# Kernel optimization log

Measured on AMD Instinct MI355X. Metric: run time of the kernel, lower is better.

## Reference

```python
import jax, jax.numpy as jnp
import numpy as np

DIM = 256
HEADS = 8
HEAD_DIM = DIM // HEADS
WS = 8
EPS = 1e-5


def layernorm(x, g, b):
    mu = jnp.mean(x, axis=-1, keepdims=True)
    var = jnp.var(x, axis=-1, keepdims=True)
    return (x - mu) * jax.lax.rsqrt(var + EPS) * g + b


def partition_windows(x, ws):
    B, H, W, C = x.shape
    x = x.reshape(B, H // ws, ws, W // ws, ws, C)
    x = jnp.transpose(x, (0, 1, 3, 2, 4, 5))
    return x.reshape(B * (H // ws) * (W // ws), ws * ws, C)


def unpartition_windows(x, ws, B, H, W):
    C = x.shape[-1]
    x = x.reshape(B, H // ws, W // ws, ws, ws, C)
    x = jnp.transpose(x, (0, 1, 3, 2, 4, 5))
    return x.reshape(B, H, W, C)


def setup_inputs() -> dict:
    key = jax.random.key(0)
    ks = jax.random.split(key, 14)
    B, H, W, C = 16, 64, 64, DIM
    s_in = 1.0 / np.sqrt(C)
    s_hid = 1.0 / np.sqrt(4 * C)
    return {
        "x": jax.random.normal(ks[0], (B, H, W, C), jnp.float32),
        "ln1_g": jnp.ones((C,), jnp.float32),
        "ln1_b": jnp.zeros((C,), jnp.float32),
        "qkv_w": jax.random.uniform(ks[1], (3 * C, C), jnp.float32, -s_in, s_in),
        "qkv_b": jax.random.uniform(ks[2], (3 * C,), jnp.float32, -s_in, s_in),
        "proj_w": jax.random.uniform(ks[3], (C, C), jnp.float32, -s_in, s_in),
        "proj_b": jax.random.uniform(ks[4], (C,), jnp.float32, -s_in, s_in),
        "ln2_g": jnp.ones((C,), jnp.float32),
        "ln2_b": jnp.zeros((C,), jnp.float32),
        "ffn_w1": jax.random.uniform(ks[5], (4 * C, C), jnp.float32, -s_in, s_in),
        "ffn_b1": jax.random.uniform(ks[6], (4 * C,), jnp.float32, -s_in, s_in),
        "ffn_w2": jax.random.uniform(ks[7], (C, 4 * C), jnp.float32, -s_hid, s_hid),
        "ffn_b2": jax.random.uniform(ks[8], (C,), jnp.float32, -s_hid, s_hid),
    }


def attention(blocks, qkv_w, qkv_b, proj_w, proj_b):
    # blocks: [Bn, N, C]
    Bn, N, C = blocks.shape
    qkv = blocks @ qkv_w.T + qkv_b  # [Bn, N, 3C]
    qkv = qkv.reshape(Bn, N, 3, HEADS, HEAD_DIM)
    q, k, v = qkv[:, :, 0], qkv[:, :, 1], qkv[:, :, 2]  # each [Bn, N, h, d]
    # Faithful to the source: q @ k^T over the last two dims -> head-x-head scores per token
    scores = jnp.einsum("bnhd,bngd->bnhg", q, k) / np.sqrt(HEAD_DIM)
    attn = jax.nn.softmax(scores, axis=-1)
    out = jnp.einsum("bnhg,bngd->bnhd", attn, v).reshape(Bn, N, C)
    return out @ proj_w.T + proj_b


def reference(x, ln1_g, ln1_b, qkv_w, qkv_b, proj_w, proj_b,
              ln2_g, ln2_b, ffn_w1, ffn_b1, ffn_w2, ffn_b2):
    B, H, W, C = x.shape
    x_ = layernorm(x, ln1_g, ln1_b)
    blocks = partition_windows(x_, WS)  # [B*nW, ws*ws, C]
    out = attention(blocks, qkv_w, qkv_b, proj_w, proj_b)
    x = x + unpartition_windows(out, WS, B, H, W)
    x_ = layernorm(x, ln2_g, ln2_b)
    x_ = jax.nn.relu(x_ @ ffn_w1.T + ffn_b1) @ ffn_w2.T + ffn_b2
    return x + x_
```

## Files before the change

### kernel.cpp

```cpp
#include <hip/hip_runtime.h>
#include <hip/hip_bf16.h>
#include <stdint.h>

typedef float f32x4 __attribute__((ext_vector_type(4)));
typedef __bf16 bf16x8 __attribute__((ext_vector_type(8)));
typedef unsigned short ushort8 __attribute__((ext_vector_type(8)));

__device__ __forceinline__ float bf2f(unsigned short u) {
    unsigned int x = ((unsigned int)u) << 16;
    return __builtin_bit_cast(float, x);
}
__device__ __forceinline__ unsigned short f2bf(float f) {
    unsigned int x = __builtin_bit_cast(unsigned int, f);
    unsigned int lsb = (x >> 16) & 1u;
    x += 0x7fffu + lsb;
    return (unsigned short)(x >> 16);
}

#define GLL16(gptr, lptr)                                                      \
    __builtin_amdgcn_global_load_lds(                                          \
        (const __attribute__((address_space(1))) void*)(gptr),                 \
        (__attribute__((address_space(3))) void*)(lptr), 16, 0, 0)

__global__ __launch_bounds__(256) void cvt4_kernel(
    const float* __restrict__ w0, const float* __restrict__ w1,
    const float* __restrict__ w2, const float* __restrict__ w3,
    unsigned short* __restrict__ dst)
{
    const int i = blockIdx.x * 256 + threadIdx.x;
    const float* s; int off;
    if      (i <  49152) { s = w0; off = 0; }
    else if (i <  65536) { s = w1; off = 49152; }
    else if (i < 131072) { s = w2; off = 65536; }
    else                 { s = w3; off = 131072; }
    f32x4 v = ((const f32x4*)s)[i - off];
    ushort4 o;
    o.x = f2bf(v.x); o.y = f2bf(v.y); o.z = f2bf(v.z); o.w = f2bf(v.w);
    ((ushort4*)dst)[i] = o;
}

__global__ __launch_bounds__(256) void ln_kernel(
    const float* __restrict__ x, const float* __restrict__ g,
    const float* __restrict__ b, unsigned short* __restrict__ y)
{
    const int lane = threadIdx.x & 63, wave = threadIdx.x >> 6;
    const size_t tok = (size_t)blockIdx.x * 4 + wave;
    f32x4 v = *(const f32x4*)(x + tok * 256 + lane * 4);
    float s = v.x + v.y + v.z + v.w;
    float q = v.x * v.x + v.y * v.y + v.z * v.z + v.w * v.w;
#pragma unroll
    for (int o = 32; o; o >>= 1) {
        s += __shfl_xor(s, o, 64);
        q += __shfl_xor(q, o, 64);
    }
    float mean = s * (1.f / 256.f);
    float var  = q * (1.f / 256.f) - mean * mean;
    float rstd = rsqrtf(var + 1e-5f);
    f32x4 gr = *(const f32x4*)(g + lane * 4);
    f32x4 br = *(const f32x4*)(b + lane * 4);
    ushort4 o4;
    o4.x = f2bf((v.x - mean) * rstd * gr.x + br.x);
    o4.y = f2bf((v.y - mean) * rstd * gr.y + br.y);
    o4.z = f2bf((v.z - mean) * rstd * gr.z + br.z);
    o4.w = f2bf((v.w - mean) * rstd * gr.w + br.w);
    *(ushort4*)(y + tok * 256 + lane * 4) = o4;
}

template <int RELU, int HASRES, int OUTF32>
__global__ __launch_bounds__(256) void gemm_bt(
    const unsigned short* __restrict__ A,
    const unsigned short* __restrict__ W,
    const float* __restrict__ bias,
    const float* res,
    void* Cv,
    int M, int N, int K, int nby)
{
    __shared__ __align__(16) unsigned short As[128 * 64];
    __shared__ __align__(16) unsigned short Bs[128 * 64];

    const int t    = threadIdx.x;
    const int id   = blockIdx.x;
    const int xcd  = id & 7;
    const int sl   = id >> 3;
    const int by   = sl % nby;
    const int bx   = (sl / nby) * 8 + xcd;
    const int m0   = bx * 128;
    const int n0   = by * 128;
    const int lane = t & 63;
    const int wave = t >> 6;
    const int wm = wave & 1, wn = wave >> 1;
    const int lr = lane & 15, kc = lane >> 4;

    f32x4 acc[4][4] = {};

    const int rA   = t >> 3;
    const int gcol = ((t & 7) ^ (rA & 7)) * 8;
    const unsigned short* gA = A + (size_t)(m0 + rA) * K + gcol;
    const unsigned short* gB = W + (size_t)(n0 + rA) * K + gcol;

    for (int k0 = 0; k0 < K; k0 += 64) {
#pragma unroll
        for (int w = 0; w < 4; ++w) {
            GLL16(gA + (size_t)(w * 32) * K + k0, &As[(w * 256 + t) * 8]);
            GLL16(gB + (size_t)(w * 32) * K + k0, &Bs[(w * 256 + t) * 8]);
        }
        __syncthreads();

#pragma unroll
        for (int hh = 0; hh < 2; ++hh) {
            bf16x8 af[4], bf[4];
#pragma unroll
            for (int i = 0; i < 4; ++i) {
                const int ra = wm * 64 + i * 16 + lr;
                const int rb = wn * 64 + i * 16 + lr;
                af[i] = *(const bf16x8*)&As[ra * 64 + ((hh * 4 + kc) ^ (ra & 7)) * 8];
                bf[i] = *(const bf16x8*)&Bs[rb * 64 + ((hh * 4 + kc) ^ (rb & 7)) * 8];
            }
#pragma unroll
            for (int i = 0; i < 4; ++i)
#pragma unroll
                for (int j = 0; j < 4; ++j)
                    acc[i][j] = __builtin_amdgcn_mfma_f32_16x16x32_bf16(
                        af[i], bf[j], acc[i][j], 0, 0, 0);
        }
        __syncthreads();
    }

    float* Cf = (float*)Cv;
    unsigned short* Cb = (unsigned short*)Cv;
    const int row0 = m0 + wm * 64;
    const int col0 = n0 + wn * 64;
    const int cl = lane & 15;
    const int rq = (lane >> 4) * 4;
#pragma unroll
    for (int i = 0; i < 4; ++i) {
#pragma unroll
        for (int j = 0; j < 4; ++j) {
            const int col = col0 + j * 16 + cl;
            const float bv = bias[col];
#pragma unroll
            for (int r = 0; r < 4; ++r) {
                const int row = row0 + i * 16 + rq + r;
                float v = acc[i][j][r] + bv;
                if (RELU) v = fmaxf(v, 0.f);
                const size_t o = (size_t)row * N + col;
                if (HASRES) v += res[o];
                if (OUTF32) Cf[o] = v;
                else        Cb[o] = f2bf(v);
            }
        }
    }
}

__global__ __launch_bounds__(512, 2) void proj_attn(
    const unsigned short* __restrict__ qkv,
    const unsigned short* __restrict__ wp,
    const float* __restrict__ bias,
    const float* __restrict__ res,
    float* __restrict__ out)
{
    __shared__ __align__(16) unsigned short U[128 * 256];
    __shared__ __align__(16) unsigned short Wk[2][16384];

    const int t = threadIdx.x;
    const int lane = t & 63, wave = t >> 6;
    const int m0 = blockIdx.x * 128;
    const int lr = lane & 15, kc = lane >> 4;
    const int cl = lane & 15, rq = (lane >> 4) * 4;
    const int wm = wave & 1, wn = wave >> 1;

    const int r2b = t >> 3;
    const int gc2 = (t & 7) ^ (r2b & 7);

    #define STAGE_WP(kc4, Wt)                                                  \
        do {                                                                   \
            _Pragma("unroll")                                                  \
            for (int j = 0; j < 4; ++j)                                        \
                GLL16(wp + (size_t)(j * 64 + r2b) * 256 + (kc4) * 64 + gc2 * 8,\
                      &(Wt)[(j * 512 + t) * 8]);                               \
        } while (0)

    STAGE_WP(0, Wk[0]);
    STAGE_WP(1, Wk[1]);

    const int h = lane >> 3, g = lane & 7;
    for (int p = 0; p < 16; ++p) {
        const int row = p * 8 + wave;
        const unsigned short* base = qkv + (size_t)(m0 + row) * 768;

        float s = 0.f;
#pragma unroll
        for (int d8 = 0; d8 < 4; ++d8) {
            ushort4 qa = *(const ushort4*)(base + h * 32 + d8 * 8);
            ushort4 qb = *(const ushort4*)(base + h * 32 + d8 * 8 + 4);
            ushort4 ka = *(const ushort4*)(base + 256 + g * 32 + d8 * 8);
            ushort4 kb = *(const ushort4*)(base + 256 + g * 32 + d8 * 8 + 4);
            s += bf2f(qa.x) * bf2f(ka.x) + bf2f(qa.y) * bf2f(ka.y)
               + bf2f(qa.z) * bf2f(ka.z) + bf2f(qa.w) * bf2f(ka.w)
               + bf2f(qb.x) * bf2f(kb.x) + bf2f(qb.y) * bf2f(kb.y)
               + bf2f(qb.z) * bf2f(kb.z) + bf2f(qb.w) * bf2f(kb.w);
        }
        s *= 0.17677669529663687f;

        float mx = s;
#pragma unroll
        for (int o = 1; o < 8; o <<= 1) mx = fmaxf(mx, __shfl_xor(mx, o, 64));
        float e = __expf(s - mx);
        float sum = e;
#pragma unroll
        for (int o = 1; o < 8; o <<= 1) sum += __shfl_xor(sum, o, 64);
        const float a = e / sum;

        float o0 = 0.f, o1 = 0.f, o2 = 0.f, o3 = 0.f;
#pragma unroll
        for (int gg = 0; gg < 8; ++gg) {
            const float ag = __shfl(a, (lane & 56) | gg, 64);
            ushort4 vv = *(const ushort4*)(base + 512 + gg * 32 + g * 4);
            o0 += ag * bf2f(vv.x);
            o1 += ag * bf2f(vv.y);
            o2 += ag * bf2f(vv.z);
            o3 += ag * bf2f(vv.w);
        }
        const int gcu = lane >> 1;
        const int sc = (gcu & ~7) | ((gcu & 7) ^ (row & 7));
        ushort4 ov;
        ov.x = f2bf(o0); ov.y = f2bf(o1); ov.z = f2bf(o2); ov.w = f2bf(o3);
        *(ushort4*)&U[row * 256 + sc * 8 + (lane & 1) * 4] = ov;
    }
    __syncthreads();

    bf16x8 afr[4][8];
#pragma unroll
    for (int i = 0; i < 4; ++i) {
        const int ra = wm * 64 + i * 16 + lr;
#pragma unroll
        for (int ks = 0; ks < 8; ++ks) {
            const int c = ks * 4 + kc;
            afr[i][ks] = *(const bf16x8*)
                &U[ra * 256 + ((c & ~7) | ((c & 7) ^ (ra & 7))) * 8];
        }
    }

    f32x4 acc[4][4] = {};
    for (int c4 = 0; c4 < 4; ++c4) {
        if (c4 >= 2) __syncthreads();
        const unsigned short* Wc = Wk[c4 & 1];
#pragma unroll
        for (int kk = 0; kk < 2; ++kk) {
            const int c = kk * 4 + kc;
            bf16x8 bw[4];
#pragma unroll
            for (int j = 0; j < 4; ++j) {
                const int rb = wn * 64 + j * 16 + lr;
                bw[j] = *(const bf16x8*)&Wc[rb * 64 + ((c ^ (rb & 7)) * 8)];
            }
#pragma unroll
            for (int i = 0; i < 4; ++i)
#pragma unroll
                for (int j = 0; j < 4; ++j)
                    acc[i][j] = __builtin_amdgcn_mfma_f32_16x16x32_bf16(
                        afr[i][c4 * 2 + kk], bw[j], acc[i][j], 0, 0, 0);
        }
        if (c4 < 2) {
            __syncthreads();
            STAGE_WP(c4 + 2, Wk[c4 & 1]);
        }
    }

#pragma unroll
    for (int i = 0; i < 4; ++i)
#pragma unroll
        for (int j = 0; j < 4; ++j) {
            const int col = wn * 64 + j * 16 + cl;
            const float bv = bias[col];
#pragma unroll
            for (int r = 0; r < 4; ++r) {
                const int row = m0 + wm * 64 + i * 16 + rq + r;
                const size_t o = (size_t)row * 256 + col;
                out[o] = acc[i][j][r] + bv + res[o];
            }
        }
    #undef STAGE_WP
}

__global__ __launch_bounds__(512, 2) void ffn_fused(
    float* xo,
    const float* __restrict__ ln2_g, const float* __restrict__ ln2_b,
    const unsigned short* __restrict__ w1,
    const float* __restrict__ b1p,
    const unsigned short* __restrict__ w2,
    const float* __restrict__ b2p)
{
    __shared__ __align__(16) unsigned short U[32768];
    __shared__ __align__(16) unsigned short W1a[16384];
    __shared__ __align__(16) unsigned short W2a[16384];
    __shared__ __align__(16) unsigned short Hs[2][8192];

    unsigned short* const W1b = U;
    unsigned short* const W2b = U + 16384;

    const int t = threadIdx.x;
    const int lane = t & 63, wave = t >> 6;
    const int m0 = blockIdx.x * 128;
    const int lr = lane & 15, kc = lane >> 4;
    const int cl = lane & 15, rq = (lane >> 4) * 4;
    const int wm = wave & 1, wn = wave >> 1;

    const int r1b = t >> 5;
    const int sc1 = t & 31;
    const int gc1 = (sc1 & ~7) | ((sc1 & 7) ^ (r1b & 7));
    const int r2b = t >> 3;
    const int gc2 = (t & 7) ^ (r2b & 7);

    #define STAGE_W1(hp, W1t)                                                  \
        do {                                                                   \
            _Pragma("unroll")                                                  \
            for (int j = 0; j < 4; ++j)                                        \
                GLL16(w1 + (size_t)((hp) * 64 + j * 16 + r1b) * 256 + gc1 * 8, \
                      &(W1t)[(j * 512 + t) * 8]);                              \
        } while (0)
    #define STAGE_W2(hp, W2t)                                                  \
        do {                                                                   \
            _Pragma("unroll")                                                  \
            for (int j = 0; j < 4; ++j)                                        \
                GLL16(w2 + (size_t)(j * 64 + r2b) * 1024 + (hp) * 64 + gc2 * 8,\
                      &(W2t)[(j * 512 + t) * 8]);                              \
        } while (0)

    STAGE_W1(0, W1a);
    STAGE_W2(0, W2a);

    {
        const int row0 = t >> 2;
        const int seg  = t & 3;
        const float* xrp = xo + (size_t)(m0 + row0) * 256 + seg * 64;
        f32x4 xv[16];
#pragma unroll
        for (int i = 0; i < 16; ++i) xv[i] = ((const f32x4*)xrp)[i];
        float s = 0.f, q = 0.f;
#pragma unroll
        for (int i = 0; i < 16; ++i) {
            s += xv[i].x + xv[i].y + xv[i].z + xv[i].w;
            q += xv[i].x * xv[i].x + xv[i].y * xv[i].y
               + xv[i].z * xv[i].z + xv[i].w * xv[i].w;
        }
        s += __shfl_xor(s, 1, 64); q += __shfl_xor(q, 1, 64);
        s += __shfl_xor(s, 2, 64); q += __shfl_xor(q, 2, 64);
        const float mean = s * (1.f / 256.f);
        const float rstd = rsqrtf(q * (1.f / 256.f) - mean * mean + 1e-5f);
#pragma unroll
        for (int c8 = 0; c8 < 8; ++c8) {
            const f32x4 g0 = ((const f32x4*)(ln2_g + seg * 64 + c8 * 8))[0];
            const f32x4 g1 = ((const f32x4*)(ln2_g + seg * 64 + c8 * 8))[1];
            const f32x4 bb0 = ((const f32x4*)(ln2_b + seg * 64 + c8 * 8))[0];
            const f32x4 bb1 = ((const f32x4*)(ln2_b + seg * 64 + c8 * 8))[1];
            const f32x4 a0 = xv[c8 * 2], a1 = xv[c8 * 2 + 1];
            ushort8 o;
            o[0] = f2bf((a0.x - mean) * rstd * g0.x + bb0.x);
            o[1] = f2bf((a0.y - mean) * rstd * g0.y + bb0.y);
            o[2] = f2bf((a0.z - mean) * rstd * g0.z + bb0.z);
            o[3] = f2bf((a0.w - mean) * rstd * g0.w + bb0.w);
            o[4] = f2bf((a1.x - mean) * rstd * g1.x + bb1.x);
            o[5] = f2bf((a1.y - mean) * rstd * g1.y + bb1.y);
            o[6] = f2bf((a1.z - mean) * rstd * g1.z + bb1.z);
            o[7] = f2bf((a1.w - mean) * rstd * g1.w + bb1.w);
            const int gc = seg * 8 + c8;
            const int sc = (gc & ~7) | ((gc & 7) ^ (row0 & 7));
            *(ushort8*)&U[row0 * 256 + sc * 8] = o;
        }
    }
    __syncthreads();

    bf16x8 afr[4][8];
#pragma unroll
    for (int i = 0; i < 4; ++i) {
        const int ra = wm * 64 + i * 16 + lr;
#pragma unroll
        for (int ks = 0; ks < 8; ++ks) {
            const int c = ks * 4 + kc;
            afr[i][ks] = *(const bf16x8*)
                &U[ra * 256 + ((c & ~7) | ((c & 7) ^ (ra & 7))) * 8];
        }
    }
    __syncthreads();
    STAGE_W1(1, W1b);

    f32x4 acc[4][4] = {};

    #define HPHASE(hcv, W1c, Hbuf)                                             \
        do {                                                                   \
            f32x4 acch[4] = {};                                                \
            __builtin_amdgcn_s_setprio(1);                                     \
            _Pragma("unroll")                                                  \
            for (int ks = 0; ks < 8; ++ks) {                                   \
                const int c = ks * 4 + kc;                                     \
                const int rb = wn * 16 + lr;                                   \
                const bf16x8 bfr = *(const bf16x8*)                            \
                    &(W1c)[rb * 256 + ((c & ~7) | ((c & 7) ^ (rb & 7))) * 8];  \
                _Pragma("unroll")                                              \
                for (int i = 0; i < 4; ++i)                                    \
                    acch[i] = __builtin_amdgcn_mfma_f32_16x16x32_bf16(         \
                        bfr, afr[i][ks], acch[i], 0, 0, 0);                    \
            }                                                                  \
            __builtin_amdgcn_s_setprio(0);                                     \
            const f32x4 bv = *(const f32x4*)(b1p + (hcv) * 64 + wn * 16 + rq); \
            const int sbase = wn * 2 + (rq >> 3);                              \
            _Pragma("unroll")                                                  \
            for (int i = 0; i < 4; ++i) {                                      \
                const int tok = wm * 64 + i * 16 + cl;                         \
                ushort4 o;                                                     \
                o.x = f2bf(fmaxf(acch[i][0] + bv.x, 0.f));                     \
                o.y = f2bf(fmaxf(acch[i][1] + bv.y, 0.f));                     \
                o.z = f2bf(fmaxf(acch[i][2] + bv.z, 0.f));                     \
                o.w = f2bf(fmaxf(acch[i][3] + bv.w, 0.f));                     \
                *(ushort4*)&(Hbuf)[tok * 64 + ((sbase ^ (tok & 7)) * 8)        \
                                   + (rq & 4)] = o;                            \
            }                                                                  \
        } while (0)

    #define OPHASE(W2c, Hbuf)                                                  \
        do {                                                                   \
            _Pragma("unroll")                                                  \
            for (int ks = 0; ks < 2; ++ks) {                                   \
                const int c = ks * 4 + kc;                                     \
                bf16x8 bw[4];                                                  \
                _Pragma("unroll")                                              \
                for (int j = 0; j < 4; ++j) {                                  \
                    const int rb = wn * 64 + j * 16 + lr;                      \
                    bw[j] = *(const bf16x8*)                                   \
                        &(W2c)[rb * 64 + ((c ^ (rb & 7)) * 8)];                \
                }                                                              \
                __builtin_amdgcn_s_setprio(1);                                 \
                _Pragma("unroll")                                              \
                for (int i = 0; i < 4; ++i) {                                  \
                    const int ra = wm * 64 + i * 16 + lr;                      \
                    const bf16x8 ah = *(const bf16x8*)                         \
                        &(Hbuf)[ra * 64 + ((c ^ (ra & 7)) * 8)];               \
                    _Pragma("unroll")                                          \
                    for (int j = 0; j < 4; ++j)                                \
                        acc[i][j] = __builtin_amdgcn_mfma_f32_16x16x32_bf16(   \
                            ah, bw[j], acc[i][j], 0, 0, 0);                    \
                }                                                              \
                __builtin_amdgcn_s_setprio(0);                                 \
            }                                                                  \
        } while (0)

    HPHASE(0, W1a, Hs[0]);
    __syncthreads();

    for (int hc = 0; hc < 16; ++hc) {
        if (hc < 14) STAGE_W1(hc + 2, (hc & 1) ? W1b : W1a);
        if (hc < 15) STAGE_W2(hc + 1, (hc & 1) ? W2a : W2b);
        if (hc < 15) HPHASE(hc + 1, (hc & 1) ? W1a : W1b, Hs[(hc + 1) & 1]);
        OPHASE((hc & 1) ? W2b : W2a, Hs[hc & 1]);
        __syncthreads();
    }

    const int rqe = (lane >> 4) * 4;
#pragma unroll
    for (int i = 0; i < 4; ++i)
#pragma unroll
        for (int j = 0; j < 4; ++j) {
            const int col = wn * 64 + j * 16 + cl;
            const float bv = b2p[col];
#pragma unroll
            for (int r = 0; r < 4; ++r) {
                const int row = m0 + wm * 64 + i * 16 + rqe + r;
                const size_t o = (size_t)row * 256 + col;
                xo[o] = acc[i][j][r] + bv + xo[o];
            }
        }
    #undef STAGE_W1
    #undef STAGE_W2
    #undef HPHASE
    #undef OPHASE
}

extern "C" void kernel_launch(void* const* d_in, const int* in_sizes, int n_in,
                              void* d_out, int out_size, void* d_ws, size_t ws_size,
                              hipStream_t stream)
{
    const float* x      = (const float*)d_in[0];
    const float* ln1_g  = (const float*)d_in[1];
    const float* ln1_b  = (const float*)d_in[2];
    const float* qkv_w  = (const float*)d_in[3];
    const float* qkv_b  = (const float*)d_in[4];
    const float* proj_w = (const float*)d_in[5];
    const float* proj_b = (const float*)d_in[6];
    const float* ln2_g  = (const float*)d_in[7];
    const float* ln2_b  = (const float*)d_in[8];
    const float* ffn_w1 = (const float*)d_in[9];
    const float* ffn_b1 = (const float*)d_in[10];
    const float* ffn_w2 = (const float*)d_in[11];
    const float* ffn_b2 = (const float*)d_in[12];
    float* xo = (float*)d_out;

    const int M = 65536;
    const size_t MEG = 1024 * 1024;
    unsigned short* ws = (unsigned short*)d_ws;
    unsigned short* qkv_wb  = ws;
    unsigned short* proj_wb = ws + 196608;
    unsigned short* ffn_w1b = ws + 262144;
    unsigned short* ffn_w2b = ws + 524288;
    unsigned short* xn   = ws + 1 * MEG;
    unsigned short* qkvb = ws + 33 * MEG;

    cvt4_kernel<<<768, 256, 0, stream>>>(qkv_w, proj_w, ffn_w1, ffn_w2, ws);

    ln_kernel<<<M / 4, 256, 0, stream>>>(x, ln1_g, ln1_b, xn);
    gemm_bt<0, 0, 0><<<3072, 256, 0, stream>>>(
        xn, qkv_wb, qkv_b, nullptr, qkvb, M, 768, 256, 6);
    proj_attn<<<M / 128, 512, 0, stream>>>(
        qkvb, proj_wb, proj_b, x, xo);
    ffn_fused<<<M / 128, 512, 0, stream>>>(
        xo, ln2_g, ln2_b, ffn_w1b, ffn_b1, ffn_w2b, ffn_b2);
}
```

Before: 343.6 us.

## Shrink LDS footprint in proj and FFN kernels to double occupancy

Both proj_attn and ffn_fused are reworked to reuse a single shared buffer for activations and weights, dropping the separate double buffers. This cuts LDS per block so launch bounds can ask for four blocks per CU instead of two. The FFN loop now runs single-buffered: compute H, sync, load the next W1, compute the output, sync, load the next W2. That adds barriers and removes the software pipelining that overlapped weight loads with MFMA work. The change relies on higher occupancy to hide latency instead, and the register cap implied by four 512-thread blocks may cause spills.

```diff
diff --git a/kernel.cpp b/kernel.cpp
--- a/kernel.cpp
+++ b/kernel.cpp
@@ -152,15 +152,17 @@
     }
 }
 
-__global__ __launch_bounds__(512, 2) void proj_attn(
+__global__ __launch_bounds__(512, 4) void proj_attn(
     const unsigned short* __restrict__ qkv,
     const unsigned short* __restrict__ wp,
     const float* __restrict__ bias,
     const float* __restrict__ res,
     float* __restrict__ out)
 {
-    __shared__ __align__(16) unsigned short U[128 * 256];
-    __shared__ __align__(16) unsigned short Wk[2][16384];
+    __shared__ __align__(16) unsigned short U[32768];
+
+    unsigned short* const UW0 = U;
+    unsigned short* const UW1 = U + 16384;
 
     const int t = threadIdx.x;
     const int lane = t & 63, wave = t >> 6;
@@ -179,9 +181,6 @@
                 GLL16(wp + (size_t)(j * 64 + r2b) * 256 + (kc4) * 64 + gc2 * 8,\
                       &(Wt)[(j * 512 + t) * 8]);                               \
         } while (0)
-
-    STAGE_WP(0, Wk[0]);
-    STAGE_WP(1, Wk[1]);
 
     const int h = lane >> 3, g = lane & 7;
     for (int p = 0; p < 16; ++p) {
@@ -240,11 +239,15 @@
                 &U[ra * 256 + ((c & ~7) | ((c & 7) ^ (ra & 7))) * 8];
         }
     }
+    __syncthreads();
+
+    STAGE_WP(0, UW0);
+    STAGE_WP(1, UW1);
+    __syncthreads();
 
     f32x4 acc[4][4] = {};
     for (int c4 = 0; c4 < 4; ++c4) {
-        if (c4 >= 2) __syncthreads();
-        const unsigned short* Wc = Wk[c4 & 1];
+        const unsigned short* Wc = (c4 & 1) ? UW1 : UW0;
 #pragma unroll
         for (int kk = 0; kk < 2; ++kk) {
             const int c = kk * 4 + kc;
@@ -261,9 +264,9 @@
                     acc[i][j] = __builtin_amdgcn_mfma_f32_16x16x32_bf16(
                         afr[i][c4 * 2 + kk], bw[j], acc[i][j], 0, 0, 0);
         }
-        if (c4 < 2) {
+        if (c4 < 3) {
             __syncthreads();
-            STAGE_WP(c4 + 2, Wk[c4 & 1]);
+            if (c4 < 2) STAGE_WP(c4 + 2, (c4 & 1) ? UW1 : UW0);
         }
     }
 
@@ -283,7 +286,7 @@
     #undef STAGE_WP
 }
 
-__global__ __launch_bounds__(512, 2) void ffn_fused(
+__global__ __launch_bounds__(512, 4) void ffn_fused(
     float* xo,
     const float* __restrict__ ln2_g, const float* __restrict__ ln2_b,
     const unsigned short* __restrict__ w1,
@@ -291,13 +294,11 @@
     const unsigned short* __restrict__ w2,
     const float* __restrict__ b2p)
 {
-    __shared__ __align__(16) unsigned short U[32768];
-    __shared__ __align__(16) unsigned short W1a[16384];
-    __shared__ __align__(16) unsigned short W2a[16384];
-    __shared__ __align__(16) unsigned short Hs[2][8192];
-
-    unsigned short* const W1b = U;
-    unsigned short* const W2b = U + 16384;
+    __shared__ __align__(16) unsigned short WB[32768];
+    __shared__ __align__(16) unsigned short Hs[8192];
+
+    unsigned short* const W1 = WB;
+    unsigned short* const W2 = WB + 16384;
 
     const int t = threadIdx.x;
     const int lane = t & 63, wave = t >> 6;
@@ -312,23 +313,20 @@
     const int r2b = t >> 3;
     const int gc2 = (t & 7) ^ (r2b & 7);
 
-    #define STAGE_W1(hp, W1t)                                                  \
+    #define STAGE_W1(hp)                                                       \
         do {                                                                   \
             _Pragma("unroll")                                                  \
             for (int j = 0; j < 4; ++j)                                        \
                 GLL16(w1 + (size_t)((hp) * 64 + j * 16 + r1b) * 256 + gc1 * 8, \
-                      &(W1t)[(j * 512 + t) * 8]);                              \
+                      &W1[(j * 512 + t) * 8]);                                 \
         } while (0)
-    #define STAGE_W2(hp, W2t)                                                  \
+    #define STAGE_W2(hp)                                                       \
         do {                                                                   \
             _Pragma("unroll")                                                  \
             for (int j = 0; j < 4; ++j)                                        \
                 GLL16(w2 + (size_t)(j * 64 + r2b) * 1024 + (hp) * 64 + gc2 * 8,\
-                      &(W2t)[(j * 512 + t) * 8]);                              \
+                      &W2[(j * 512 + t) * 8]);                                 \
         } while (0)
-
-    STAGE_W1(0, W1a);
-    STAGE_W2(0, W2a);
 
     {
         const int row0 = t >> 2;
@@ -366,7 +364,7 @@
             o[7] = f2bf((a1.w - mean) * rstd * g1.w + bb1.w);
             const int gc = seg * 8 + c8;
             const int sc = (gc & ~7) | ((gc & 7) ^ (row0 & 7));
-            *(ushort8*)&U[row0 * 256 + sc * 8] = o;
+            *(ushort8*)&WB[row0 * 256 + sc * 8] = o;
         }
     }
     __syncthreads();
@@ -379,15 +377,18 @@
         for (int ks = 0; ks < 8; ++ks) {
             const int c = ks * 4 + kc;
             afr[i][ks] = *(const bf16x8*)
-                &U[ra * 256 + ((c & ~7) | ((c & 7) ^ (ra & 7))) * 8];
+                &WB[ra * 256 + ((c & ~7) | ((c & 7) ^ (ra & 7))) * 8];
         }
     }
     __syncthreads();
-    STAGE_W1(1, W1b);
+
+    STAGE_W1(0);
+    STAGE_W2(0);
+    __syncthreads();
 
     f32x4 acc[4][4] = {};
 
-    #define HPHASE(hcv, W1c, Hbuf)                                             \
+    #define HPHASE(hcv)                                                        \
         do {                                                                   \
             f32x4 acch[4] = {};                                                \
             __builtin_amdgcn_s_setprio(1);                                     \
@@ -396,7 +397,7 @@
                 const int c = ks * 4 + kc;                                     \
                 const int rb = wn * 16 + lr;                                   \
                 const bf16x8 bfr = *(const bf16x8*)                            \
-                    &(W1c)[rb * 256 + ((c & ~7) | ((c & 7) ^ (rb & 7))) * 8];  \
+                    &W1[rb * 256 + ((c & ~7) | ((c & 7) ^ (rb & 7))) * 8];     \
                 _Pragma("unroll")                                              \
                 for (int i = 0; i < 4; ++i)                                    \
                     acch[i] = __builtin_amdgcn_mfma_f32_16x16x32_bf16(         \
@@ -413,12 +414,12 @@
                 o.y = f2bf(fmaxf(acch[i][1] + bv.y, 0.f));                     \
                 o.z = f2bf(fmaxf(acch[i][2] + bv.z, 0.f));                     \
                 o.w = f2bf(fmaxf(acch[i][3] + bv.w, 0.f));                     \
-                *(ushort4*)&(Hbuf)[tok * 64 + ((sbase ^ (tok & 7)) * 8)        \
-                                   + (rq & 4)] = o;                            \
+                *(ushort4*)&Hs[tok * 64 + ((sbase ^ (tok & 7)) * 8)            \
+                               + (rq & 4)] = o;                                \
             }                                                                  \
         } while (0)
 
-    #define OPHASE(W2c, Hbuf)                                                  \
+    #define OPHASE()                                                           \
         do {                                                                   \
             _Pragma("unroll")                                                  \
             for (int ks = 0; ks < 2; ++ks) {                                   \
@@ -428,14 +429,14 @@
                 for (int j = 0; j < 4; ++j) {                                  \
                     const int rb = wn * 64 + j * 16 + lr;                      \
                     bw[j] = *(const bf16x8*)                                   \
-                        &(W2c)[rb * 64 + ((c ^ (rb & 7)) * 8)];                \
+                        &W2[rb * 64 + ((c ^ (rb & 7)) * 8)];                   \
                 }                                                              \
                 __builtin_amdgcn_s_setprio(1);                                 \
                 _Pragma("unroll")                                              \
                 for (int i = 0; i < 4; ++i) {                                  \
                     const int ra = wm * 64 + i * 16 + lr;                      \
                     const bf16x8 ah = *(const bf16x8*)                         \
-                        &(Hbuf)[ra * 64 + ((c ^ (ra & 7)) * 8)];               \
+                        &Hs[ra * 64 + ((c ^ (ra & 7)) * 8)];                   \
                     _Pragma("unroll")                                          \
                     for (int j = 0; j < 4; ++j)                                \
                         acc[i][j] = __builtin_amdgcn_mfma_f32_16x16x32_bf16(   \
@@ -445,15 +446,13 @@
             }                                                                  \
         } while (0)
 
-    HPHASE(0, W1a, Hs[0]);
-    __syncthreads();
-
     for (int hc = 0; hc < 16; ++hc) {
-        if (hc < 14) STAGE_W1(hc + 2, (hc & 1) ? W1b : W1a);
-        if (hc < 15) STAGE_W2(hc + 1, (hc & 1) ? W2a : W2b);
-        if (hc < 15) HPHASE(hc + 1, (hc & 1) ? W1a : W1b, Hs[(hc + 1) & 1]);
-        OPHASE((hc & 1) ? W2b : W2a, Hs[hc & 1]);
+        HPHASE(hc);
         __syncthreads();
+        if (hc < 15) STAGE_W1(hc + 1);
+        OPHASE();
+        __syncthreads();
+        if (hc < 15) STAGE_W2(hc + 1);
     }
 
     const int rqe = (lane >> 4) * 4;
```

After: 594.9 us. 73.1% more time.

## Fuse LayerNorm1 into QKV GEMM with register-resident A fragments

Applied to the files above, without the earlier changes.

Replaces the separate LayerNorm kernel and the generic tiled QKV GEMM with one kernel. Each block normalizes 128 tokens into LDS, loads all A fragments into registers, then streams 64-column slices of the QKV weight through double-buffered LDS and writes bf16 QKV with bias. This removes the bf16 normalized-activation round trip through global memory and one launch. In exchange it uses many registers per thread and narrower per-iteration MFMA work, with a barrier between each weight slice.

```diff
diff --git a/kernel.cpp b/kernel.cpp
--- a/kernel.cpp
+++ b/kernel.cpp
@@ -39,117 +39,130 @@
     ((ushort4*)dst)[i] = o;
 }
 
-__global__ __launch_bounds__(256) void ln_kernel(
-    const float* __restrict__ x, const float* __restrict__ g,
-    const float* __restrict__ b, unsigned short* __restrict__ y)
+__global__ __launch_bounds__(512, 2) void qkv_ln(
+    const float* __restrict__ x,
+    const float* __restrict__ ln_g, const float* __restrict__ ln_b,
+    const unsigned short* __restrict__ wq,
+    const float* __restrict__ qb,
+    unsigned short* __restrict__ qkvb)
 {
-    const int lane = threadIdx.x & 63, wave = threadIdx.x >> 6;
-    const size_t tok = (size_t)blockIdx.x * 4 + wave;
-    f32x4 v = *(const f32x4*)(x + tok * 256 + lane * 4);
-    float s = v.x + v.y + v.z + v.w;
-    float q = v.x * v.x + v.y * v.y + v.z * v.z + v.w * v.w;
-#pragma unroll
-    for (int o = 32; o; o >>= 1) {
-        s += __shfl_xor(s, o, 64);
-        q += __shfl_xor(q, o, 64);
-    }
-    float mean = s * (1.f / 256.f);
-    float var  = q * (1.f / 256.f) - mean * mean;
-    float rstd = rsqrtf(var + 1e-5f);
-    f32x4 gr = *(const f32x4*)(g + lane * 4);
-    f32x4 br = *(const f32x4*)(b + lane * 4);
-    ushort4 o4;
-    o4.x = f2bf((v.x - mean) * rstd * gr.x + br.x);
-    o4.y = f2bf((v.y - mean) * rstd * gr.y + br.y);
-    o4.z = f2bf((v.z - mean) * rstd * gr.z + br.z);
-    o4.w = f2bf((v.w - mean) * rstd * gr.w + br.w);
-    *(ushort4*)(y + tok * 256 + lane * 4) = o4;
-}
-
-template <int RELU, int HASRES, int OUTF32>
-__global__ __launch_bounds__(256) void gemm_bt(
-    const unsigned short* __restrict__ A,
-    const unsigned short* __restrict__ W,
-    const float* __restrict__ bias,
-    const float* res,
-    void* Cv,
-    int M, int N, int K, int nby)
-{
-    __shared__ __align__(16) unsigned short As[128 * 64];
-    __shared__ __align__(16) unsigned short Bs[128 * 64];
-
-    const int t    = threadIdx.x;
-    const int id   = blockIdx.x;
-    const int xcd  = id & 7;
-    const int sl   = id >> 3;
-    const int by   = sl % nby;
-    const int bx   = (sl / nby) * 8 + xcd;
-    const int m0   = bx * 128;
-    const int n0   = by * 128;
-    const int lane = t & 63;
-    const int wave = t >> 6;
+    __shared__ __align__(16) unsigned short U[32768];
+    unsigned short* const U0 = U;
+    unsigned short* const U1 = U + 16384;
+
+    const int t = threadIdx.x;
+    const int lane = t & 63, wave = t >> 6;
+    const int m0 = blockIdx.x * 128;
+    const int lr = lane & 15, kc = lane >> 4;
+    const int cl = lane & 15, rq = (lane >> 4) * 4;
     const int wm = wave & 1, wn = wave >> 1;
-    const int lr = lane & 15, kc = lane >> 4;
-
-    f32x4 acc[4][4] = {};
-
-    const int rA   = t >> 3;
-    const int gcol = ((t & 7) ^ (rA & 7)) * 8;
-    const unsigned short* gA = A + (size_t)(m0 + rA) * K + gcol;
-    const unsigned short* gB = W + (size_t)(n0 + rA) * K + gcol;
-
-    for (int k0 = 0; k0 < K; k0 += 64) {
-#pragma unroll
-        for (int w = 0; w < 4; ++w) {
-            GLL16(gA + (size_t)(w * 32) * K + k0, &As[(w * 256 + t) * 8]);
-            GLL16(gB + (size_t)(w * 32) * K + k0, &Bs[(w * 256 + t) * 8]);
-        }
-        __syncthreads();
-
-#pragma unroll
-        for (int hh = 0; hh < 2; ++hh) {
-            bf16x8 af[4], bf[4];
+
+    const int r1b = t >> 5;
+    const int sc1 = t & 31;
+    const int gc1 = (sc1 & ~7) | ((sc1 & 7) ^ (r1b & 7));
+
+    #define STAGE_W(hs, Wt)                                                    \
+        do {                                                                   \
+            _Pragma("unroll")                                                  \
+            for (int j = 0; j < 4; ++j)                                        \
+                GLL16(wq + (size_t)((hs) * 64 + j * 16 + r1b) * 256 + gc1 * 8, \
+                      &(Wt)[(j * 512 + t) * 8]);                               \
+        } while (0)
+
+    {
+        const int row0 = t >> 2;
+        const int seg  = t & 3;
+        const float* xrp = x + (size_t)(m0 + row0) * 256 + seg * 64;
+        f32x4 xv[16];
+#pragma unroll
+        for (int i = 0; i < 16; ++i) xv[i] = ((const f32x4*)xrp)[i];
+        float s = 0.f, q = 0.f;
+#pragma unroll
+        for (int i = 0; i < 16; ++i) {
+            s += xv[i].x + xv[i].y + xv[i].z + xv[i].w;
+            q += xv[i].x * xv[i].x + xv[i].y * xv[i].y
+               + xv[i].z * xv[i].z + xv[i].w * xv[i].w;
+        }
+        s += __shfl_xor(s, 1, 64); q += __shfl_xor(q, 1, 64);
+        s += __shfl_xor(s, 2, 64); q += __shfl_xor(q, 2, 64);
+        const float mean = s * (1.f / 256.f);
+        const float rstd = rsqrtf(q * (1.f / 256.f) - mean * mean + 1e-5f);
+#pragma unroll
+        for (int c8 = 0; c8 < 8; ++c8) {
+            const f32x4 g0 = ((const f32x4*)(ln_g + seg * 64 + c8 * 8))[0];
+            const f32x4 g1 = ((const f32x4*)(ln_g + seg * 64 + c8 * 8))[1];
+            const f32x4 bb0 = ((const f32x4*)(ln_b + seg * 64 + c8 * 8))[0];
+            const f32x4 bb1 = ((const f32x4*)(ln_b + seg * 64 + c8 * 8))[1];
+            const f32x4 a0 = xv[c8 * 2], a1 = xv[c8 * 2 + 1];
+            ushort8 o;
+            o[0] = f2bf((a0.x - mean) * rstd * g0.x + bb0.x);
+            o[1] = f2bf((a0.y - mean) * rstd * g0.y + bb0.y);
+            o[2] = f2bf((a0.z - mean) * rstd * g0.z + bb0.z);
+            o[3] = f2bf((a0.w - mean) * rstd * g0.w + bb0.w);
+            o[4] = f2bf((a1.x - mean) * rstd * g1.x + bb1.x);
+            o[5] = f2bf((a1.y - mean) * rstd * g1.y + bb1.y);
+            o[6] = f2bf((a1.z - mean) * rstd * g1.z + bb1.z);
+            o[7] = f2bf((a1.w - mean) * rstd * g1.w + bb1.w);
+            const int gc = seg * 8 + c8;
+            const int sc = (gc & ~7) | ((gc & 7) ^ (row0 & 7));
+            *(ushort8*)&U[row0 * 256 + sc * 8] = o;
+        }
+    }
+    __syncthreads();
+
+    bf16x8 afr[4][8];
+#pragma unroll
+    for (int i = 0; i < 4; ++i) {
+        const int ra = wm * 64 + i * 16 + lr;
+#pragma unroll
+        for (int ks = 0; ks < 8; ++ks) {
+            const int c = ks * 4 + kc;
+            afr[i][ks] = *(const bf16x8*)
+                &U[ra * 256 + ((c & ~7) | ((c & 7) ^ (ra & 7))) * 8];
+        }
+    }
+    __syncthreads();
+
+    STAGE_W(0, U0);
+    STAGE_W(1, U1);
+    __syncthreads();
+
+    for (int hs = 0; hs < 12; ++hs) {
+        const unsigned short* Wc = (hs & 1) ? U1 : U0;
+        f32x4 acch[4] = {};
+        __builtin_amdgcn_s_setprio(1);
+#pragma unroll
+        for (int ks = 0; ks < 8; ++ks) {
+            const int c = ks * 4 + kc;
+            const int rb = wn * 16 + lr;
+            const bf16x8 bfr = *(const bf16x8*)
+                &Wc[rb * 256 + ((c & ~7) | ((c & 7) ^ (rb & 7))) * 8];
+#pragma unroll
+            for (int i = 0; i < 4; ++i)
+                acch[i] = __builtin_amdgcn_mfma_f32_16x16x32_bf16(
+                    bfr, afr[i][ks], acch[i], 0, 0, 0);
+        }
+        __builtin_amdgcn_s_setprio(0);
+        {
+            const f32x4 bv = *(const f32x4*)(qb + hs * 64 + wn * 16 + rq);
+            const int colb = hs * 64 + wn * 16 + rq;
 #pragma unroll
             for (int i = 0; i < 4; ++i) {
-                const int ra = wm * 64 + i * 16 + lr;
-                const int rb = wn * 64 + i * 16 + lr;
-                af[i] = *(const bf16x8*)&As[ra * 64 + ((hh * 4 + kc) ^ (ra & 7)) * 8];
-                bf[i] = *(const bf16x8*)&Bs[rb * 64 + ((hh * 4 + kc) ^ (rb & 7)) * 8];
+                const int tok = m0 + wm * 64 + i * 16 + cl;
+                ushort4 o;
+                o.x = f2bf(acch[i][0] + bv.x);
+                o.y = f2bf(acch[i][1] + bv.y);
+                o.z = f2bf(acch[i][2] + bv.z);
+                o.w = f2bf(acch[i][3] + bv.w);
+                *(ushort4*)&qkvb[(size_t)tok * 768 + colb] = o;
             }
-#pragma unroll
-            for (int i = 0; i < 4; ++i)
-#pragma unroll
-                for (int j = 0; j < 4; ++j)
-                    acc[i][j] = __builtin_amdgcn_mfma_f32_16x16x32_bf16(
-                        af[i], bf[j], acc[i][j], 0, 0, 0);
-        }
-        __syncthreads();
-    }
-
-    float* Cf = (float*)Cv;
-    unsigned short* Cb = (unsigned short*)Cv;
-    const int row0 = m0 + wm * 64;
-    const int col0 = n0 + wn * 64;
-    const int cl = lane & 15;
-    const int rq = (lane >> 4) * 4;
-#pragma unroll
-    for (int i = 0; i < 4; ++i) {
-#pragma unroll
-        for (int j = 0; j < 4; ++j) {
-            const int col = col0 + j * 16 + cl;
-            const float bv = bias[col];
-#pragma unroll
-            for (int r = 0; r < 4; ++r) {
-                const int row = row0 + i * 16 + rq + r;
-                float v = acc[i][j][r] + bv;
-                if (RELU) v = fmaxf(v, 0.f);
-                const size_t o = (size_t)row * N + col;
-                if (HASRES) v += res[o];
-                if (OUTF32) Cf[o] = v;
-                else        Cb[o] = f2bf(v);
-            }
-        }
-    }
+        }
+        if (hs < 11) {
+            __syncthreads();
+            if (hs < 10) STAGE_W(hs + 2, (hs & 1) ? U1 : U0);
+        }
+    }
+    #undef STAGE_W
 }
 
 __global__ __launch_bounds__(512, 2) void proj_attn(
@@ -502,14 +515,12 @@
     unsigned short* proj_wb = ws + 196608;
     unsigned short* ffn_w1b = ws + 262144;
     unsigned short* ffn_w2b = ws + 524288;
-    unsigned short* xn   = ws + 1 * MEG;
     unsigned short* qkvb = ws + 33 * MEG;
 
     cvt4_kernel<<<768, 256, 0, stream>>>(qkv_w, proj_w, ffn_w1, ffn_w2, ws);
 
-    ln_kernel<<<M / 4, 256, 0, stream>>>(x, ln1_g, ln1_b, xn);
-    gemm_bt<0, 0, 0><<<3072, 256, 0, stream>>>(
-        xn, qkv_wb, qkv_b, nullptr, qkvb, M, 768, 256, 6);
+    qkv_ln<<<M / 128, 512, 0, stream>>>(
+        x, ln1_g, ln1_b, qkv_wb, qkv_b, qkvb);
     proj_attn<<<M / 128, 512, 0, stream>>>(
         qkvb, proj_wb, proj_b, x, xo);
     ffn_fused<<<M / 128, 512, 0, stream>>>(
```

Result: no change. 347.0 us (+1.0%).
